# Kernel tuning notes

Measured on AMD Instinct MI355X. Metric: run time of the kernel, lower is better.

The kernel has to match this reference:

```python
import jax, jax.numpy as jnp
import numpy as np

N = 50000   # nodes
E = 800000  # edges (sparse adjacency nnz)
FI = 256    # input feature dim
FO = 64     # output feature dim per head
H = 8       # attention heads


def setup_inputs() -> dict:
    key = jax.random.key(0)
    ks = jax.random.split(key, 6)
    x = jax.random.normal(ks[0], (N, FI), dtype=jnp.float32)
    W = jax.random.normal(ks[1], (H, FI, FO), dtype=jnp.float32) * 0.05
    a = jax.random.normal(ks[2], (H, FO), dtype=jnp.float32) * 0.05
    b = jax.random.normal(ks[3], (H, FO), dtype=jnp.float32) * 0.05
    rows = jax.random.randint(ks[4], (E,), 0, N, dtype=jnp.int32)
    cols = jax.random.randint(ks[5], (E,), 0, N, dtype=jnp.int32)
    return {"x": x, "W": W, "a": a, "b": b, "rows": rows, "cols": cols}


def reference(x, W, a, b, rows, cols):
    # SparseGAT forward: per head linear -> edge scores -> sparse row softmax
    # -> sparse aggregation -> bias; heads averaged then ReLU.
    n = x.shape[0]
    h = W.shape[0]
    NEG_SLOPE = 0.2  # tf.nn.leaky_relu default alpha
    acc = None
    for i in range(h):  # small fixed loop over heads
        t = x @ W[i]                                   # [N, FO]
        aw = t @ a[i]                                  # [N]
        e = jax.nn.leaky_relu(aw[rows] + aw[cols], NEG_SLOPE)   # [E]
        # sparse softmax per row (segment softmax, numerically stable)
        m = jax.ops.segment_max(e, rows, num_segments=n)        # [N]
        ex = jnp.exp(e - m[rows])                                # [E]
        den = jax.ops.segment_sum(ex, rows, num_segments=n)      # [N]
        coef = ex / den[rows]                                    # [E]
        # sparse matmul: sum_j coef_ij * t_j
        agg = jax.ops.segment_sum(coef[:, None] * t[cols], rows, num_segments=n)
        agg = agg + b[i]
        acc = agg if acc is None else acc + agg
    return jax.nn.relu(acc / h)
```

## Files before the change

### kernel.cpp

```cpp
#include <hip/hip_runtime.h>
#include <hip/hip_bf16.h>
#include <hip/hip_fp16.h>


#define FI 256
#define FO 64
#define NH 8
#define FC 512
#define BM 64
#define NBIN 64

typedef _Float16 f16x8 __attribute__((ext_vector_type(8)));
typedef float f32x16 __attribute__((ext_vector_type(16)));
typedef float f32x8 __attribute__((ext_vector_type(8)));

__global__ __launch_bounds__(256)
void prep(const float* __restrict__ W, _Float16* __restrict__ Wth,
          int* __restrict__ zbase, int zints, int zb) {
  const int t = threadIdx.x;
  if ((int)blockIdx.x < zb) {
    int i = blockIdx.x * 256 + t;
    if (i * 4 < zints)
      reinterpret_cast<int4*>(zbase)[i] = make_int4(0, 0, 0, 0);
  } else {
    int idx = (blockIdx.x - zb) * 256 + t;
    if (idx < NH * FO * FI) {
      int k = idx & (FI - 1);
      int f = (idx >> 8) & (FO - 1);
      int h = idx >> 14;
      Wth[idx] = (_Float16)W[((size_t)h * FI + k) * FO + f];
    }
  }
}

__global__ __launch_bounds__(512)
void k1b1(const float* __restrict__ x, const _Float16* __restrict__ Wth,
          const float* __restrict__ a, _Float16* __restrict__ Th,
          float* __restrict__ aw, int N, int kb,
          const int* __restrict__ rows, int* __restrict__ deg, int E) {
  if ((int)blockIdx.x >= kb) {
    int e = (blockIdx.x - kb) * 512 + threadIdx.x;
    if (e < E) atomicAdd(&deg[rows[e]], 1);
    return;
  }

  __shared__ _Float16 Xs[BM][136];
  const int bm = blockIdx.x * BM;
  const int t = threadIdx.x;
  const int w = t >> 6;
  const int lane = t & 63;
  const int l31 = lane & 31;
  const int hi = lane >> 5;
  const int kh = hi * 8;
  const _Float16* Wh = Wth + (size_t)w * (FO * FI);

  f32x16 acc[2][2];
  #pragma unroll
  for (int mr = 0; mr < 2; ++mr)
    #pragma unroll
    for (int wc = 0; wc < 2; ++wc) acc[mr][wc] = (f32x16)0.0f;

  #pragma unroll
  for (int k0 = 0; k0 < 2; ++k0) {
    if (k0) __syncthreads();
    #pragma unroll
    for (int r = 0; r < 4; ++r) {
      int i = t + r * 512;
      int row = i >> 5;
      int q = i & 31;
      float4 v = make_float4(0.f, 0.f, 0.f, 0.f);
      if (bm + row < N)
        v = reinterpret_cast<const float4*>(&x[(size_t)(bm + row) * FI + k0 * 128])[q];
      _Float16 o[4] = {(_Float16)v.x, (_Float16)v.y, (_Float16)v.z, (_Float16)v.w};
      *reinterpret_cast<uint2*>(&Xs[row][q * 4]) = *reinterpret_cast<uint2*>(o);
    }
    __syncthreads();
    #pragma unroll
    for (int kk = 0; kk < 8; ++kk) {
      f16x8 xf[2], wf[2];
      #pragma unroll
      for (int mr = 0; mr < 2; ++mr)
        xf[mr] = *reinterpret_cast<const f16x8*>(&Xs[mr * 32 + l31][kk * 16 + kh]);
      #pragma unroll
      for (int wc = 0; wc < 2; ++wc)
        wf[wc] = *reinterpret_cast<const f16x8*>(
            &Wh[(size_t)(wc * 32 + l31) * FI + k0 * 128 + kk * 16 + kh]);
      #pragma unroll
      for (int mr = 0; mr < 2; ++mr)
        #pragma unroll
        for (int wc = 0; wc < 2; ++wc)
          acc[mr][wc] =
              __builtin_amdgcn_mfma_f32_32x32x16_f16(wf[wc], xf[mr], acc[mr][wc], 0, 0, 0);
    }
  }

  float s4[2] = {0.f, 0.f};
  #pragma unroll
  for (int wc = 0; wc < 2; ++wc)
    #pragma unroll
    for (int reg = 0; reg < 16; ++reg) {
      float av = a[w * FO + wc * 32 + (reg & 3) + 8 * (reg >> 2) + 4 * hi];
      #pragma unroll
      for (int mr = 0; mr < 2; ++mr)
        s4[mr] = fmaf(acc[mr][wc][reg], av, s4[mr]);
    }
  #pragma unroll
  for (int mr = 0; mr < 2; ++mr) {
    float s = s4[mr] + __shfl_xor(s4[mr], 32);
    int n = bm + mr * 32 + l31;
    if (hi == 0 && n < N) aw[(size_t)n * NH + w] = s;
  }

  #pragma unroll
  for (int mr = 0; mr < 2; ++mr) {
    int n = bm + mr * 32 + l31;
    if (n >= N) continue;
    _Float16* rowp = Th + (size_t)n * FC + w * FO;
    #pragma unroll
    for (int wc = 0; wc < 2; ++wc)
      #pragma unroll
      for (int g = 0; g < 4; ++g) {
        _Float16 o[4] = {(_Float16)acc[mr][wc][4 * g + 0],
                         (_Float16)acc[mr][wc][4 * g + 1],
                         (_Float16)acc[mr][wc][4 * g + 2],
                         (_Float16)acc[mr][wc][4 * g + 3]};
        *reinterpret_cast<uint2*>(&rowp[wc * 32 + 8 * g + 4 * hi]) =
            *reinterpret_cast<uint2*>(o);
      }
  }
}

__global__ __launch_bounds__(256)
void b2a_blocksum(const int* __restrict__ deg, int* __restrict__ blocksums,
                  int* __restrict__ blockhist, int N, int nbp) {
  __shared__ int red[256];
  __shared__ int hist[NBIN];
  const int t = threadIdx.x;
  const int base = blockIdx.x * 1024 + t * 4;
  if (t < NBIN) hist[t] = 0;
  int v[4]; int s = 0;
  #pragma unroll
  for (int j = 0; j < 4; ++j) { int i = base + j; v[j] = (i < N) ? deg[i] : 0; s += v[j]; }
  __syncthreads();
  #pragma unroll
  for (int j = 0; j < 4; ++j)
    if (base + j < N) atomicAdd(&hist[min(v[j], NBIN - 1)], 1);
  red[t] = s;
  __syncthreads();
  for (int off = 128; off; off >>= 1) {
    if (t < off) red[t] += red[t + off];
    __syncthreads();
  }
  if (t == 0) blocksums[blockIdx.x] = red[0];
  if (t < NBIN) blockhist[t * nbp + blockIdx.x] = hist[t];
}

__global__ __launch_bounds__(128)
void b2b5b_scan(int* __restrict__ blocksums, int nb,
                int* __restrict__ row_start, int N, int E,
                int* __restrict__ blockhist, int nbp) {
  const int w = threadIdx.x >> 6;
  const int lane = threadIdx.x & 63;
  if (w == 0) {
    int carry = 0;
    for (int base = 0; base < nb; base += 64) {
      int i = base + lane;
      int v = (i < nb) ? blocksums[i] : 0;
      int inc = v;
      #pragma unroll
      for (int off = 1; off < 64; off <<= 1) {
        int t = __shfl_up(inc, off);
        if (lane >= off) inc += t;
      }
      if (i < nb) blocksums[i] = inc - v + carry;
      carry += __shfl(inc, 63);
    }
    if (lane == 0) row_start[N] = E;
  } else {
    int* rowp = blockhist + (size_t)(NBIN - 1 - lane) * nbp;
    int tot = 0;
    for (int c = 0; c < nbp / 4; ++c) {
      int4 v = reinterpret_cast<const int4*>(rowp)[c];
      tot += v.x + v.y + v.z + v.w;
    }
    int inc = tot;
    #pragma unroll
    for (int off = 1; off < 64; off <<= 1) {
      int t = __shfl_up(inc, off);
      if (lane >= off) inc += t;
    }
    int run = inc - tot;
    for (int c = 0; c < nbp / 4; ++c) {
      int4 v = reinterpret_cast<const int4*>(rowp)[c];
      int4 o;
      o.x = run; run += v.x;
      o.y = run; run += v.y;
      o.z = run; run += v.z;
      o.w = run; run += v.w;
      reinterpret_cast<int4*>(rowp)[c] = o;
    }
  }
}

__global__ __launch_bounds__(256)
void b2c_rescan(const int* __restrict__ deg, const int* __restrict__ blocksums,
                int* __restrict__ row_start, int* __restrict__ cursor, int N) {
  __shared__ int ts[256];
  const int t = threadIdx.x;
  const int base = blockIdx.x * 1024 + t * 4;
  int v[4]; int s = 0;
  #pragma unroll
  for (int j = 0; j < 4; ++j) { int i = base + j; v[j] = (i < N) ? deg[i] : 0; s += v[j]; }
  ts[t] = s;
  __syncthreads();
  for (int off = 1; off < 256; off <<= 1) {
    int add = (t >= off) ? ts[t - off] : 0;
    __syncthreads();
    ts[t] += add;
    __syncthreads();
  }
  int run = blocksums[blockIdx.x] + ts[t] - s;
  #pragma unroll
  for (int j = 0; j < 4; ++j) {
    int i = base + j;
    if (i < N) { row_start[i] = run; cursor[i] = run; run += v[j]; }
  }
}

__global__ __launch_bounds__(256)
void b3b5c_scatter(const int* __restrict__ rows, const int* __restrict__ cols,
                   int* __restrict__ cursor, int* __restrict__ colperm, int E,
                   const int* __restrict__ deg, const int* __restrict__ blockhist,
                   int* __restrict__ row_order, int N, int nbp, int nb) {
  __shared__ int cur[NBIN];
  const int t = threadIdx.x;
  if ((int)blockIdx.x < nb) {
    if (t < NBIN) cur[t] = blockhist[t * nbp + blockIdx.x];
    __syncthreads();
    const int base = blockIdx.x * 1024 + t * 4;
    #pragma unroll
    for (int j = 0; j < 4; ++j) {
      int i = base + j;
      if (i < N) {
        int pos = atomicAdd(&cur[min(deg[i], NBIN - 1)], 1);
        row_order[pos] = i;
      }
    }
  } else {
    int e = (blockIdx.x - nb) * 256 + t;
    if (e < E) {
      int pos = atomicAdd(&cursor[rows[e]], 1);
      colperm[pos] = cols[e];
    }
  }
}

__global__ __launch_bounds__(256)
void k4_fused(const int* __restrict__ row_start, const int* __restrict__ colperm,
              const int* __restrict__ row_order,
              const float* __restrict__ aw, const _Float16* __restrict__ Th,
              const float* __restrict__ b, float* __restrict__ out, int N) {
  const int lane16 = threadIdx.x & 15;
  const int gbase  = threadIdx.x & 48;
  const int hi8    = lane16 >> 3;
  const int ri = blockIdx.x * 16 + (threadIdx.x >> 4);
  if (ri >= N) return;
  const int r = row_order[ri];

  const int s0 = row_start[r], s1 = row_start[r + 1];
  f32x8 awr = *reinterpret_cast<const f32x8*>(&aw[(size_t)r * NH]);

  float facc[4][8] = {};
  float dacc[NH] = {};

  for (int base = s0; base < s1; base += 16) {
    const int mm = min(16, s1 - base);
    const bool valid = lane16 < mm;

    int key = valid ? colperm[base + lane16] : 0x7fffffff;
    #pragma unroll
    for (int k = 2; k <= 16; k <<= 1)
      #pragma unroll
      for (int j = k >> 1; j > 0; j >>= 1) {
        int other = __shfl_xor(key, j);
        bool take_min = (((lane16 & k) == 0) == ((lane16 & j) == 0));
        key = take_min ? min(key, other) : max(key, other);
      }
    int c_l = valid ? key : 0;

    f32x8 awc = *reinterpret_cast<const f32x8*>(&aw[(size_t)c_l * NH]);
    float ex[NH];
    int pkv[4];
    #pragma unroll
    for (int h = 0; h < NH; ++h) {
      float s = awr[h] + awc[h];
      float lr = s > 0.f ? s : 0.2f * s;
      ex[h] = valid ? __expf(lr) : 0.f;
      dacc[h] += ex[h];
    }
    #pragma unroll
    for (int q = 0; q < 4; ++q) {
      __half2 h2 = __floats2half2_rn(ex[2 * q], ex[2 * q + 1]);
      pkv[q] = *reinterpret_cast<int*>(&h2);
    }

    for (int j = 0; j < mm; ++j) {
      int cj = __shfl(c_l, gbase + j);
      const _Float16* tp = Th + (size_t)cj * FC + lane16 * 8;
      f16x8 tv0 = *reinterpret_cast<const f16x8*>(tp);
      f16x8 tv1 = *reinterpret_cast<const f16x8*>(tp + 128);
      f16x8 tv2 = *reinterpret_cast<const f16x8*>(tp + 256);
      f16x8 tv3 = *reinterpret_cast<const f16x8*>(tp + 384);
      float eq[4];
      #pragma unroll
      for (int q = 0; q < 4; ++q) {
        int p = __shfl(pkv[q], gbase + j);
        float2 f2 = __half22float2(*reinterpret_cast<__half2*>(&p));
        eq[q] = hi8 ? f2.y : f2.x;
      }
      #pragma unroll
      for (int e = 0; e < 8; ++e) {
        facc[0][e] = fmaf(eq[0], (float)tv0[e], facc[0][e]);
        facc[1][e] = fmaf(eq[1], (float)tv1[e], facc[1][e]);
        facc[2][e] = fmaf(eq[2], (float)tv2[e], facc[2][e]);
        facc[3][e] = fmaf(eq[3], (float)tv3[e], facc[3][e]);
      }
    }
  }

  #pragma unroll
  for (int h = 0; h < NH; ++h) {
    #pragma unroll
    for (int off = 1; off < 16; off <<= 1)
      dacc[h] += __shfl_xor(dacc[h], off);
  }
  float rden[NH];
  #pragma unroll
  for (int h = 0; h < NH; ++h) rden[h] = dacc[h] > 0.f ? 1.0f / dacc[h] : 0.f;

  float s[8] = {};
  #pragma unroll
  for (int q = 0; q < 4; ++q) {
    float rd = hi8 ? rden[2 * q + 1] : rden[2 * q];
    #pragma unroll
    for (int e = 0; e < 8; ++e) s[e] = fmaf(facc[q][e], rd, s[e]);
  }
  #pragma unroll
  for (int e = 0; e < 8; ++e) s[e] += __shfl_xor(s[e], 8);

  if (lane16 < 8) {
    #pragma unroll
    for (int e = 0; e < 8; ++e) {
      const int f = lane16 * 8 + e;
      float sb = 0.f;
      #pragma unroll
      for (int h = 0; h < NH; ++h) sb += b[h * FO + f];
      float v = (s[e] + sb) * 0.125f;
      out[(size_t)r * FO + f] = v > 0.f ? v : 0.f;
    }
  }
}

extern "C" void kernel_launch(void* const* d_in, const int* in_sizes, int n_in,
                              void* d_out, int out_size, void* d_ws, size_t ws_size,
                              hipStream_t stream) {
  const float* x    = (const float*)d_in[0];
  const float* W    = (const float*)d_in[1];
  const float* a    = (const float*)d_in[2];
  const float* b    = (const float*)d_in[3];
  const int*   rows = (const int*)d_in[4];
  const int*   cols = (const int*)d_in[5];
  const int N = in_sizes[0] / FI;
  const int E = in_sizes[4];

  const int nb  = (N + 1023) / 1024;
  const int nbp = ((nb + 3) / 4) * 4;

  char* p = (char*)d_ws;
  _Float16* Th       = (_Float16*)p;  p += (size_t)N * FC * sizeof(_Float16);
  _Float16* Wth      = (_Float16*)p;  p += (size_t)NH * FO * FI * sizeof(_Float16);
  float*    aw       = (float*)p;     p += (size_t)N * NH * sizeof(float);
  int*      deg      = (int*)p;       p += (size_t)N * sizeof(int);
  int*      blockhist= (int*)p;       p += (size_t)NBIN * nbp * sizeof(int);
  int*      row_start= (int*)p;       p += (size_t)(N + 4) * sizeof(int);
  int*      cursor   = (int*)p;       p += (size_t)N * sizeof(int);
  int*      colperm  = (int*)p;       p += (size_t)E * sizeof(int);
  int*      blocksums= (int*)p;       p += 64 * sizeof(int);
  int*      row_order= (int*)p;       p += (size_t)N * sizeof(int);
  float*    out = (float*)d_out;

  const int zints = N + NBIN * nbp;
  const int zb = (zints / 4 + 255) / 256;
  const int pb = (NH * FO * FI + 255) / 256;
  prep<<<zb + pb, 256, 0, stream>>>(W, Wth, deg, zints, zb);

  const int kb = (N + BM - 1) / BM;
  const int hb = (E + 511) / 512;
  k1b1<<<kb + hb, 512, 0, stream>>>(x, Wth, a, Th, aw, N, kb, rows, deg, E);

  b2a_blocksum<<<nb, 256, 0, stream>>>(deg, blocksums, blockhist, N, nbp);
  b2b5b_scan<<<1, 128, 0, stream>>>(blocksums, nb, row_start, N, E, blockhist, nbp);
  b2c_rescan<<<nb, 256, 0, stream>>>(deg, blocksums, row_start, cursor, N);
  b3b5c_scatter<<<nb + (E + 255) / 256, 256, 0, stream>>>(
      rows, cols, cursor, colperm, E, deg, blockhist, row_order, N, nbp, nb);

  k4_fused<<<(N + 15) / 16, 256, 0, stream>>>(row_start, colperm, row_order,
                                              aw, Th, b, out, N);
}
```

Measured before the change: 254.1 us.

## Fuse CSR build kernels into one cooperative kernel with grid syncs

Replaces four separate launches (block sum plus histogram, scan, rescan, scatter) with a single cooperative kernel of 256 blocks that separates the phases with grid.sync(). The goal is to remove the launch overhead and inter-kernel gaps of the small CSR-construction stages. The cost is three grid-wide barriers, a single block doing the scan while the others wait, and an edge scatter that now loops over 256 blocks instead of launching one thread per edge. The scatter therefore has less parallelism.

After: 352.7 us. 38.8% more time.

```diff
diff --git a/kernel.cpp b/kernel.cpp
--- a/kernel.cpp
+++ b/kernel.cpp
@@ -1,6 +1,9 @@
 #include <hip/hip_runtime.h>
 #include <hip/hip_bf16.h>
 #include <hip/hip_fp16.h>
+#include <hip/hip_cooperative_groups.h>
+
+namespace cg = cooperative_groups;
 
 
 #define FI 256
@@ -131,127 +134,121 @@
 }
 
 __global__ __launch_bounds__(256)
-void b2a_blocksum(const int* __restrict__ deg, int* __restrict__ blocksums,
-                  int* __restrict__ blockhist, int N, int nbp) {
-  __shared__ int red[256];
+void csrcoop(const int* __restrict__ deg, int* __restrict__ blocksums,
+             int* __restrict__ blockhist, int* __restrict__ row_start,
+             int* __restrict__ cursor, const int* __restrict__ rows,
+             const int* __restrict__ cols, int* __restrict__ colperm,
+             int* __restrict__ row_order, int N, int E, int nb, int nbp) {
+  cg::grid_group grid = cg::this_grid();
+  const int t = threadIdx.x;
+  const int vb = blockIdx.x;
+  __shared__ int ts[256];
   __shared__ int hist[NBIN];
-  const int t = threadIdx.x;
-  const int base = blockIdx.x * 1024 + t * 4;
-  if (t < NBIN) hist[t] = 0;
-  int v[4]; int s = 0;
-  #pragma unroll
-  for (int j = 0; j < 4; ++j) { int i = base + j; v[j] = (i < N) ? deg[i] : 0; s += v[j]; }
-  __syncthreads();
-  #pragma unroll
-  for (int j = 0; j < 4; ++j)
-    if (base + j < N) atomicAdd(&hist[min(v[j], NBIN - 1)], 1);
-  red[t] = s;
-  __syncthreads();
-  for (int off = 128; off; off >>= 1) {
-    if (t < off) red[t] += red[t + off];
+
+  if (vb < nb) {
+    if (t < NBIN) hist[t] = 0;
+    const int base = vb * 1024 + t * 4;
+    int v[4]; int s = 0;
+    #pragma unroll
+    for (int j = 0; j < 4; ++j) { int i = base + j; v[j] = (i < N) ? deg[i] : 0; s += v[j]; }
     __syncthreads();
-  }
-  if (t == 0) blocksums[blockIdx.x] = red[0];
-  if (t < NBIN) blockhist[t * nbp + blockIdx.x] = hist[t];
-}
-
-__global__ __launch_bounds__(128)
-void b2b5b_scan(int* __restrict__ blocksums, int nb,
-                int* __restrict__ row_start, int N, int E,
-                int* __restrict__ blockhist, int nbp) {
-  const int w = threadIdx.x >> 6;
-  const int lane = threadIdx.x & 63;
-  if (w == 0) {
-    int carry = 0;
-    for (int base = 0; base < nb; base += 64) {
-      int i = base + lane;
-      int v = (i < nb) ? blocksums[i] : 0;
-      int inc = v;
+    #pragma unroll
+    for (int j = 0; j < 4; ++j)
+      if (base + j < N) atomicAdd(&hist[min(v[j], NBIN - 1)], 1);
+    ts[t] = s;
+    __syncthreads();
+    for (int off = 128; off; off >>= 1) {
+      if (t < off) ts[t] += ts[t + off];
+      __syncthreads();
+    }
+    if (t == 0) blocksums[vb] = ts[0];
+    if (t < NBIN) blockhist[t * nbp + vb] = hist[t];
+  }
+  grid.sync();
+
+  if (vb == 0 && t < 128) {
+    const int w = t >> 6;
+    const int lane = t & 63;
+    if (w == 0) {
+      int carry = 0;
+      for (int base = 0; base < nb; base += 64) {
+        int i = base + lane;
+        int v = (i < nb) ? blocksums[i] : 0;
+        int inc = v;
+        #pragma unroll
+        for (int off = 1; off < 64; off <<= 1) {
+          int tt = __shfl_up(inc, off);
+          if (lane >= off) inc += tt;
+        }
+        if (i < nb) blocksums[i] = inc - v + carry;
+        carry += __shfl(inc, 63);
+      }
+      if (lane == 0) row_start[N] = E;
+    } else {
+      int* rowp = blockhist + (size_t)(NBIN - 1 - lane) * nbp;
+      int tot = 0;
+      for (int c = 0; c < nbp / 4; ++c) {
+        int4 v = reinterpret_cast<const int4*>(rowp)[c];
+        tot += v.x + v.y + v.z + v.w;
+      }
+      int inc = tot;
       #pragma unroll
       for (int off = 1; off < 64; off <<= 1) {
-        int t = __shfl_up(inc, off);
-        if (lane >= off) inc += t;
-      }
-      if (i < nb) blocksums[i] = inc - v + carry;
-      carry += __shfl(inc, 63);
-    }
-    if (lane == 0) row_start[N] = E;
-  } else {
-    int* rowp = blockhist + (size_t)(NBIN - 1 - lane) * nbp;
-    int tot = 0;
-    for (int c = 0; c < nbp / 4; ++c) {
-      int4 v = reinterpret_cast<const int4*>(rowp)[c];
-      tot += v.x + v.y + v.z + v.w;
-    }
-    int inc = tot;
-    #pragma unroll
-    for (int off = 1; off < 64; off <<= 1) {
-      int t = __shfl_up(inc, off);
-      if (lane >= off) inc += t;
-    }
-    int run = inc - tot;
-    for (int c = 0; c < nbp / 4; ++c) {
-      int4 v = reinterpret_cast<const int4*>(rowp)[c];
-      int4 o;
-      o.x = run; run += v.x;
-      o.y = run; run += v.y;
-      o.z = run; run += v.z;
-      o.w = run; run += v.w;
-      reinterpret_cast<int4*>(rowp)[c] = o;
-    }
-  }
-}
-
-__global__ __launch_bounds__(256)
-void b2c_rescan(const int* __restrict__ deg, const int* __restrict__ blocksums,
-                int* __restrict__ row_start, int* __restrict__ cursor, int N) {
-  __shared__ int ts[256];
-  const int t = threadIdx.x;
-  const int base = blockIdx.x * 1024 + t * 4;
-  int v[4]; int s = 0;
-  #pragma unroll
-  for (int j = 0; j < 4; ++j) { int i = base + j; v[j] = (i < N) ? deg[i] : 0; s += v[j]; }
-  ts[t] = s;
-  __syncthreads();
-  for (int off = 1; off < 256; off <<= 1) {
-    int add = (t >= off) ? ts[t - off] : 0;
+        int tt = __shfl_up(inc, off);
+        if (lane >= off) inc += tt;
+      }
+      int run = inc - tot;
+      for (int c = 0; c < nbp / 4; ++c) {
+        int4 v = reinterpret_cast<const int4*>(rowp)[c];
+        int4 o;
+        o.x = run; run += v.x;
+        o.y = run; run += v.y;
+        o.z = run; run += v.z;
+        o.w = run; run += v.w;
+        reinterpret_cast<int4*>(rowp)[c] = o;
+      }
+    }
+  }
+  grid.sync();
+
+  if (vb < nb) {
+    const int base = vb * 1024 + t * 4;
+    int v[4]; int s = 0;
+    #pragma unroll
+    for (int j = 0; j < 4; ++j) { int i = base + j; v[j] = (i < N) ? deg[i] : 0; s += v[j]; }
+    ts[t] = s;
     __syncthreads();
-    ts[t] += add;
+    for (int off = 1; off < 256; off <<= 1) {
+      int add = (t >= off) ? ts[t - off] : 0;
+      __syncthreads();
+      ts[t] += add;
+      __syncthreads();
+    }
+    int run = blocksums[vb] + ts[t] - s;
+    #pragma unroll
+    for (int j = 0; j < 4; ++j) {
+      int i = base + j;
+      if (i < N) { row_start[i] = run; cursor[i] = run; run += v[j]; }
+    }
+  }
+  grid.sync();
+
+  if (vb < nb) {
+    if (t < NBIN) hist[t] = blockhist[t * nbp + vb];
     __syncthreads();
-  }
-  int run = blocksums[blockIdx.x] + ts[t] - s;
-  #pragma unroll
-  for (int j = 0; j < 4; ++j) {
-    int i = base + j;
-    if (i < N) { row_start[i] = run; cursor[i] = run; run += v[j]; }
-  }
-}
-
-__global__ __launch_bounds__(256)
-void b3b5c_scatter(const int* __restrict__ rows, const int* __restrict__ cols,
-                   int* __restrict__ cursor, int* __restrict__ colperm, int E,
-                   const int* __restrict__ deg, const int* __restrict__ blockhist,
-                   int* __restrict__ row_order, int N, int nbp, int nb) {
-  __shared__ int cur[NBIN];
-  const int t = threadIdx.x;
-  if ((int)blockIdx.x < nb) {
-    if (t < NBIN) cur[t] = blockhist[t * nbp + blockIdx.x];
-    __syncthreads();
-    const int base = blockIdx.x * 1024 + t * 4;
+    const int base = vb * 1024 + t * 4;
     #pragma unroll
     for (int j = 0; j < 4; ++j) {
       int i = base + j;
       if (i < N) {
-        int pos = atomicAdd(&cur[min(deg[i], NBIN - 1)], 1);
+        int pos = atomicAdd(&hist[min(deg[i], NBIN - 1)], 1);
         row_order[pos] = i;
       }
     }
-  } else {
-    int e = (blockIdx.x - nb) * 256 + t;
-    if (e < E) {
-      int pos = atomicAdd(&cursor[rows[e]], 1);
-      colperm[pos] = cols[e];
-    }
+  }
+  for (int e = vb * 256 + t; e < E; e += gridDim.x * 256) {
+    int pos = atomicAdd(&cursor[rows[e]], 1);
+    colperm[pos] = cols[e];
   }
 }
 
@@ -398,11 +395,18 @@
   const int hb = (E + 511) / 512;
   k1b1<<<kb + hb, 512, 0, stream>>>(x, Wth, a, Th, aw, N, kb, rows, deg, E);
 
-  b2a_blocksum<<<nb, 256, 0, stream>>>(deg, blocksums, blockhist, N, nbp);
-  b2b5b_scan<<<1, 128, 0, stream>>>(blocksums, nb, row_start, N, E, blockhist, nbp);
-  b2c_rescan<<<nb, 256, 0, stream>>>(deg, blocksums, row_start, cursor, N);
-  b3b5c_scatter<<<nb + (E + 255) / 256, 256, 0, stream>>>(
-      rows, cols, cursor, colperm, E, deg, blockhist, row_order, N, nbp, nb);
+  {
+    int* deg_c = deg; int* bs_c = blocksums; int* bh_c = blockhist;
+    int* rs_c = row_start; int* cu_c = cursor;
+    const int* rw_c = rows; const int* cl_c = cols;
+    int* cp_c = colperm; int* ro_c = row_order;
+    int N_c = N, E_c = E, nb_c = nb, nbp_c = nbp;
+    void* args[] = {&deg_c, &bs_c, &bh_c, &rs_c, &cu_c,
+                    &rw_c, &cl_c, &cp_c, &ro_c,
+                    &N_c, &E_c, &nb_c, &nbp_c};
+    hipLaunchCooperativeKernel(reinterpret_cast<void*>(csrcoop),
+                               dim3(256), dim3(256), args, 0, stream);
+  }
 
   k4_fused<<<(N + 15) / 16, 256, 0, stream>>>(row_start, colperm, row_order,
                                               aw, Th, b, out, N);
```
